# Performance work log

Measured on AMD Instinct MI355X. Metric: run time of the kernel, lower is better.

## Reference

```python
import jax, jax.numpy as jnp
import numpy as np

B, I, O, T, L = 16, 512, 512, 256, 4096
EPS = 1e-8


def setup_inputs() -> dict:
    key = jax.random.key(0)
    ks = jax.random.split(key, 10)
    def lin_w(k, out_d, in_d):  # kaiming-uniform-ish init like torch Linear
        bound = 1.0 / np.sqrt(in_d)
        return jax.random.uniform(k, (out_d, in_d), jnp.float32, -bound, bound)
    return {
        "x": jax.random.normal(ks[0], (B, I, L), jnp.float32),
        "t": jax.random.normal(ks[1], (B, T), jnp.float32),
        "weight": lin_w(ks[2], O, I),            # base conv weight [O, I]
        "W1": lin_w(ks[3], T, T), "b1": jnp.zeros((T,), jnp.float32),
        "W2": lin_w(ks[4], T, T), "b2": jnp.zeros((T,), jnp.float32),
        "W3": lin_w(ks[5], I, T), "b3": jnp.zeros((I,), jnp.float32),
    }


def reference(x, t, weight, W1, b1, W2, b2, W3, b3):
    # mod MLP: Linear -> SiLU -> Linear -> SiLU -> Linear
    h = jax.nn.silu(t @ W1.T + b1)
    h = jax.nn.silu(h @ W2.T + b2)
    s = h @ W3.T + b3 + 1.0                    # [B, I] modulation scales
    bw = weight[None, :, :] * s[:, None, :]    # [B, O, I]
    demod = jax.lax.rsqrt(jnp.sum(bw * bw, axis=2) + EPS)  # [B, O]
    bw = bw * demod[:, :, None]                # demodulated per-sample weights
    # grouped 1x1 conv (groups=B) == batched pointwise contraction
    return jnp.einsum('boi,bil->bol', bw, x)   # [B, O, L]
```

## Files before the change

kernel.cpp:

```cpp
#include <hip/hip_runtime.h>
#include <hip/hip_bf16.h>

typedef float f4v __attribute__((ext_vector_type(4)));
typedef float f32x4 __attribute__((ext_vector_type(4)));
typedef __bf16 bf16x8 __attribute__((ext_vector_type(8)));

#define GLDS16(gsrc, ldst)                                                  \
  __builtin_amdgcn_global_load_lds(                                         \
      (const __attribute__((address_space(1))) unsigned int*)(gsrc),        \
      (__attribute__((address_space(3))) unsigned int*)(ldst), 16, 0, 0)

__device__ __forceinline__ unsigned pack2bf(float lo, float hi) {
  unsigned short ua = __builtin_bit_cast(unsigned short, (__bf16)lo);
  unsigned short ub = __builtin_bit_cast(unsigned short, (__bf16)hi);
  return (unsigned)ua | ((unsigned)ub << 16);
}

__global__ __launch_bounds__(256) void mlp_kernel(
    const float* __restrict__ t,
    const float* __restrict__ W1, const float* __restrict__ b1,
    const float* __restrict__ W2, const float* __restrict__ b2,
    const float* __restrict__ W3, const float* __restrict__ b3,
    float* __restrict__ s_out) {
  __shared__ float tt[256];
  __shared__ float hh[256];
  const int b = blockIdx.x;
  const int tid = threadIdx.x;
  tt[tid] = t[b * 256 + tid];
  __syncthreads();
  float acc = b1[tid];
  {
    const f4v* wrow = (const f4v*)(W1 + tid * 256);
    #pragma unroll 16
    for (int k = 0; k < 64; ++k) {
      f4v wv = wrow[k];
      acc += wv[0] * tt[4 * k] + wv[1] * tt[4 * k + 1] +
             wv[2] * tt[4 * k + 2] + wv[3] * tt[4 * k + 3];
    }
  }
  float h = acc / (1.0f + expf(-acc));
  __syncthreads();
  hh[tid] = h;
  __syncthreads();
  acc = b2[tid];
  {
    const f4v* wrow = (const f4v*)(W2 + tid * 256);
    #pragma unroll 16
    for (int k = 0; k < 64; ++k) {
      f4v wv = wrow[k];
      acc += wv[0] * hh[4 * k] + wv[1] * hh[4 * k + 1] +
             wv[2] * hh[4 * k + 2] + wv[3] * hh[4 * k + 3];
    }
  }
  h = acc / (1.0f + expf(-acc));
  __syncthreads();
  tt[tid] = h;
  __syncthreads();
  #pragma unroll
  for (int rep = 0; rep < 2; ++rep) {
    const int o = rep * 256 + tid;
    float a3 = b3[o];
    const f4v* wrow = (const f4v*)(W3 + o * 256);
    #pragma unroll 16
    for (int k = 0; k < 64; ++k) {
      f4v wv = wrow[k];
      a3 += wv[0] * tt[4 * k] + wv[1] * tt[4 * k + 1] +
            wv[2] * tt[4 * k + 2] + wv[3] * tt[4 * k + 3];
    }
    s_out[b * 512 + o] = a3 + 1.0f;
  }
}

__global__ __launch_bounds__(256) void modw_kernel(
    const float* __restrict__ weight, const float* __restrict__ s_in,
    unsigned short* __restrict__ bwq) {
  const int tid = threadIdx.x;
  const int wid = (blockIdx.x << 2) | (tid >> 6);
  const int b = wid >> 9;
  const int o = wid & 511;
  const int lane = tid & 63;
  const f4v* wp = (const f4v*)(weight + o * 512 + lane * 8);
  const f4v* sp = (const f4v*)(s_in + b * 512 + lane * 8);
  f4v w0 = wp[0], w1 = wp[1];
  f4v s0 = sp[0], s1 = sp[1];
  float p[8];
  p[0] = w0[0] * s0[0]; p[1] = w0[1] * s0[1];
  p[2] = w0[2] * s0[2]; p[3] = w0[3] * s0[3];
  p[4] = w1[0] * s1[0]; p[5] = w1[1] * s1[1];
  p[6] = w1[2] * s1[2]; p[7] = w1[3] * s1[3];
  float ss = 0.0f;
  #pragma unroll
  for (int i = 0; i < 8; ++i) ss += p[i] * p[i];
  #pragma unroll
  for (int off = 32; off; off >>= 1) ss += __shfl_xor(ss, off);
  const float d = rsqrtf(ss + 1e-8f);
  uint4 outw;
  outw.x = pack2bf(p[0] * d, p[1] * d);
  outw.y = pack2bf(p[2] * d, p[3] * d);
  outw.z = pack2bf(p[4] * d, p[5] * d);
  outw.w = pack2bf(p[6] * d, p[7] * d);
  *(uint4*)(bwq + ((size_t)(b * 512 + o)) * 512 + lane * 8) = outw;
}

__global__ __launch_bounds__(256, 3) void gemm_kernel(
    const float* __restrict__ x, const unsigned short* __restrict__ bwq,
    float* __restrict__ out) {
  __shared__ __align__(16) unsigned short As[3][128 * 32];
  __shared__ __align__(16) unsigned short Bs[2][128 * 32];

  const int bid = blockIdx.x;
  const int swz = ((bid & 7) << 8) | (bid >> 3);
  const int mt = swz & 3;
  const int nt = (swz >> 2) & 31;
  const int bb = swz >> 7;

  const int tid = threadIdx.x;
  const int lane = tid & 63;
  const int wv = tid >> 6;
  const int wr = wv >> 1, wc = wv & 1;

  const unsigned short* abase = bwq + ((size_t)(bb * 512 + mt * 128)) * 512;
  const float* xbase = x + ((size_t)bb * 512) * 4096 + nt * 128;

  const int pq = tid >> 5;
  const int lc = tid & 31;
  const float* xp = xbase + (size_t)(pq * 4) * 4096 + lc * 4;
  const int sw_w = (lc & 3) << 4;
  char* BsB = (char*)Bs;

  const int g0 = tid, g1 = 256 + tid;
  const unsigned short* asrc0 = abase + (g0 >> 2) * 512 + (g0 & 3) * 8;
  const unsigned short* asrc1 = abase + (g1 >> 2) * 512 + (g1 & 3) * 8;

  const int arow = wr * 64 + (lane & 15);
  const int kgo = (lane >> 4) * 8;
  const int nrow0 = wc * 64 + (lane & 15);
  const int sb = (nrow0 >> 2) & 3;
  const int bByte = nrow0 * 64 + (((lane >> 4) ^ sb) << 4);

  f32x4 acc[4][4] = {};
  f4v xv[3][4];

#define LOADX(SET, STEP)                                                    \
  do {                                                                      \
    const float* _p = xp + (size_t)((STEP) * 32) * 4096;                    \
    xv[SET][0] = *(const f4v*)(_p);                                         \
    xv[SET][1] = *(const f4v*)(_p + 4096);                                  \
    xv[SET][2] = *(const f4v*)(_p + 8192);                                  \
    xv[SET][3] = *(const f4v*)(_p + 12288);                                 \
  } while (0)

#define STAGEA(STEP, BUF)                                                   \
  do {                                                                      \
    GLDS16(asrc0 + (STEP) * 32, &As[BUF][g0 * 8]);                          \
    GLDS16(asrc1 + (STEP) * 32, &As[BUF][g1 * 8]);                          \
  } while (0)

#define PACKB(SET, BUF)                                                     \
  do {                                                                      \
    char* _bs = BsB + (BUF) * 8192;                                         \
    _Pragma("unroll")                                                       \
    for (int j = 0; j < 4; ++j) {                                           \
      uint2 val;                                                            \
      val.x = pack2bf(xv[SET][0][j], xv[SET][1][j]);                        \
      val.y = pack2bf(xv[SET][2][j], xv[SET][3][j]);                        \
      const int n = (lc << 2) + j;                                          \
      *(uint2*)(_bs + n * 64 + ((pq * 8) ^ sw_w)) = val;                    \
    }                                                                       \
  } while (0)

#define FENCE() asm volatile("" ::: "memory")
#define BARN(N)                                                             \
  do {                                                                      \
    asm volatile("s_waitcnt lgkmcnt(0)\n\ts_waitcnt vmcnt(" #N ")" :::      \
                     "memory");                                             \
    __builtin_amdgcn_s_barrier();                                           \
    asm volatile("" ::: "memory");                                          \
  } while (0)

#define COMPUTE(CA, CB)                                                     \
  do {                                                                      \
    const unsigned short* ab = &As[CA][0];                                  \
    const char* bbuf = BsB + (CB) * 8192;                                   \
    bf16x8 a0 = *(const bf16x8*)(ab + arow * 32 + kgo);                     \
    bf16x8 a1 = *(const bf16x8*)(ab + arow * 32 + 512 + kgo);               \
    bf16x8 a2 = *(const bf16x8*)(ab + arow * 32 + 1024 + kgo);              \
    bf16x8 a3 = *(const bf16x8*)(ab + arow * 32 + 1536 + kgo);              \
    bf16x8 bf0 = *(const bf16x8*)(bbuf + bByte);                            \
    bf16x8 bf1 = *(const bf16x8*)(bbuf + bByte + 1024);                     \
    bf16x8 bf2 = *(const bf16x8*)(bbuf + bByte + 2048);                     \
    bf16x8 bf3 = *(const bf16x8*)(bbuf + bByte + 3072);                     \
    acc[0][0] = __builtin_amdgcn_mfma_f32_16x16x32_bf16(a0, bf0, acc[0][0], 0, 0, 0); \
    acc[0][1] = __builtin_amdgcn_mfma_f32_16x16x32_bf16(a0, bf1, acc[0][1], 0, 0, 0); \
    acc[0][2] = __builtin_amdgcn_mfma_f32_16x16x32_bf16(a0, bf2, acc[0][2], 0, 0, 0); \
    acc[0][3] = __builtin_amdgcn_mfma_f32_16x16x32_bf16(a0, bf3, acc[0][3], 0, 0, 0); \
    acc[1][0] = __builtin_amdgcn_mfma_f32_16x16x32_bf16(a1, bf0, acc[1][0], 0, 0, 0); \
    acc[1][1] = __builtin_amdgcn_mfma_f32_16x16x32_bf16(a1, bf1, acc[1][1], 0, 0, 0); \
    acc[1][2] = __builtin_amdgcn_mfma_f32_16x16x32_bf16(a1, bf2, acc[1][2], 0, 0, 0); \
    acc[1][3] = __builtin_amdgcn_mfma_f32_16x16x32_bf16(a1, bf3, acc[1][3], 0, 0, 0); \
    acc[2][0] = __builtin_amdgcn_mfma_f32_16x16x32_bf16(a2, bf0, acc[2][0], 0, 0, 0); \
    acc[2][1] = __builtin_amdgcn_mfma_f32_16x16x32_bf16(a2, bf1, acc[2][1], 0, 0, 0); \
    acc[2][2] = __builtin_amdgcn_mfma_f32_16x16x32_bf16(a2, bf2, acc[2][2], 0, 0, 0); \
    acc[2][3] = __builtin_amdgcn_mfma_f32_16x16x32_bf16(a2, bf3, acc[2][3], 0, 0, 0); \
    acc[3][0] = __builtin_amdgcn_mfma_f32_16x16x32_bf16(a3, bf0, acc[3][0], 0, 0, 0); \
    acc[3][1] = __builtin_amdgcn_mfma_f32_16x16x32_bf16(a3, bf1, acc[3][1], 0, 0, 0); \
    acc[3][2] = __builtin_amdgcn_mfma_f32_16x16x32_bf16(a3, bf2, acc[3][2], 0, 0, 0); \
    acc[3][3] = __builtin_amdgcn_mfma_f32_16x16x32_bf16(a3, bf3, acc[3][3], 0, 0, 0); \
  } while (0)

  STAGEA(0, 0);
  FENCE();
  LOADX(0, 0);
  STAGEA(1, 1);
  FENCE();
  LOADX(1, 1);
  LOADX(2, 2);
  PACKB(0, 0);
  BARN(10);

  #pragma unroll
  for (int it = 0; it < 16; ++it) {
    if (it <= 14) PACKB((it + 1) % 3, (it + 1) & 1);
    if (it <= 13) STAGEA(it + 2, (it + 2) % 3);
    FENCE();
    if (it <= 12) LOADX(it % 3, it + 3);
    COMPUTE(it % 3, it & 1);
    if (it <= 12) {
      BARN(10);
    } else if (it == 13) {
      BARN(6);
    } else if (it == 14) {
      BARN(0);
    }
  }

  const size_t ob =
      ((size_t)(bb * 512 + mt * 128 + wr * 64 + ((lane >> 4) << 2))) * 4096 +
      nt * 128 + wc * 64 + (lane & 15);
  #pragma unroll
  for (int mi = 0; mi < 4; ++mi)
    #pragma unroll
    for (int ni = 0; ni < 4; ++ni)
      #pragma unroll
      for (int jj = 0; jj < 4; ++jj)
        out[ob + (size_t)(mi * 16 + jj) * 4096 + ni * 16] = acc[mi][ni][jj];

#undef LOADX
#undef STAGEA
#undef PACKB
#undef FENCE
#undef BARN
#undef COMPUTE
}

extern "C" void kernel_launch(void* const* d_in, const int* in_sizes, int n_in,
                              void* d_out, int out_size, void* d_ws, size_t ws_size,
                              hipStream_t stream) {
  const float* x      = (const float*)d_in[0];
  const float* t      = (const float*)d_in[1];
  const float* weight = (const float*)d_in[2];
  const float* W1     = (const float*)d_in[3];
  const float* b1     = (const float*)d_in[4];
  const float* W2     = (const float*)d_in[5];
  const float* b2     = (const float*)d_in[6];
  const float* W3     = (const float*)d_in[7];
  const float* b3     = (const float*)d_in[8];
  float* out = (float*)d_out;

  float* s_ws = (float*)d_ws;
  unsigned short* bwq = (unsigned short*)((char*)d_ws + 32 * 1024);

  mlp_kernel<<<16, 256, 0, stream>>>(t, W1, b1, W2, b2, W3, b3, s_ws);
  modw_kernel<<<2048, 256, 0, stream>>>(weight, s_ws, bwq);
  gemm_kernel<<<2048, 256, 0, stream>>>(x, bwq, out);
}
```

Before: 126.4 us.

## Restructure GEMM pipeline with rotating LDS pointers and two-set register prefetch

Replaces the fully unrolled 16-step loop with a 7-iteration, twice-unrolled loop that rotates three A-tile LDS pointers and ping-pongs two named register sets of x values, plus a two-step tail. The hand-tuned vmcnt waits are removed. Barriers now wait only on lgkmcnt and add a sched_barrier, so the compiler has to place the global-load waits itself. The occupancy hint in launch_bounds is also dropped. The aim is less register pressure and code size, but prefetch depth for x falls from three steps to two. Correctness for the asynchronous LDS DMA of A now rests on waits the compiler inserts.

```diff
diff --git a/kernel.cpp b/kernel.cpp
--- a/kernel.cpp
+++ b/kernel.cpp
@@ -102,11 +102,11 @@
   *(uint4*)(bwq + ((size_t)(b * 512 + o)) * 512 + lane * 8) = outw;
 }
 
-__global__ __launch_bounds__(256, 3) void gemm_kernel(
+__global__ __launch_bounds__(256) void gemm_kernel(
     const float* __restrict__ x, const unsigned short* __restrict__ bwq,
     float* __restrict__ out) {
-  __shared__ __align__(16) unsigned short As[3][128 * 32];
-  __shared__ __align__(16) unsigned short Bs[2][128 * 32];
+  __shared__ __align__(16) unsigned short AsBuf[3][128 * 32];
+  __shared__ __align__(16) unsigned short BsBuf[2][128 * 32];
 
   const int bid = blockIdx.x;
   const int swz = ((bid & 7) << 8) | (bid >> 3);
@@ -126,11 +126,12 @@
   const int lc = tid & 31;
   const float* xp = xbase + (size_t)(pq * 4) * 4096 + lc * 4;
   const int sw_w = (lc & 3) << 4;
-  char* BsB = (char*)Bs;
 
   const int g0 = tid, g1 = 256 + tid;
   const unsigned short* asrc0 = abase + (g0 >> 2) * 512 + (g0 & 3) * 8;
   const unsigned short* asrc1 = abase + (g1 >> 2) * 512 + (g1 & 3) * 8;
+  const int aoff0 = g0 * 8;
+  const int aoff1 = g1 * 8;
 
   const int arow = wr * 64 + (lane & 15);
   const int kgo = (lane >> 4) * 8;
@@ -139,57 +140,60 @@
   const int bByte = nrow0 * 64 + (((lane >> 4) ^ sb) << 4);
 
   f32x4 acc[4][4] = {};
-  f4v xv[3][4];
-
-#define LOADX(SET, STEP)                                                    \
+
+  f4v xa0, xa1, xa2, xa3, xb0, xb1, xb2, xb3;
+
+  unsigned short* pA0 = &AsBuf[0][0];
+  unsigned short* pA1 = &AsBuf[1][0];
+  unsigned short* pA2 = &AsBuf[2][0];
+  char* bs0 = (char*)&BsBuf[0][0];
+  char* bs1 = (char*)&BsBuf[1][0];
+
+#define LOADX(R0, R1, R2, R3, STEP)                                         \
   do {                                                                      \
     const float* _p = xp + (size_t)((STEP) * 32) * 4096;                    \
-    xv[SET][0] = *(const f4v*)(_p);                                         \
-    xv[SET][1] = *(const f4v*)(_p + 4096);                                  \
-    xv[SET][2] = *(const f4v*)(_p + 8192);                                  \
-    xv[SET][3] = *(const f4v*)(_p + 12288);                                 \
-  } while (0)
-
-#define STAGEA(STEP, BUF)                                                   \
-  do {                                                                      \
-    GLDS16(asrc0 + (STEP) * 32, &As[BUF][g0 * 8]);                          \
-    GLDS16(asrc1 + (STEP) * 32, &As[BUF][g1 * 8]);                          \
-  } while (0)
-
-#define PACKB(SET, BUF)                                                     \
-  do {                                                                      \
-    char* _bs = BsB + (BUF) * 8192;                                         \
+    R0 = *(const f4v*)(_p);                                                 \
+    R1 = *(const f4v*)(_p + 4096);                                          \
+    R2 = *(const f4v*)(_p + 8192);                                          \
+    R3 = *(const f4v*)(_p + 12288);                                         \
+  } while (0)
+
+#define STAGEA(STEP, PDST)                                                  \
+  do {                                                                      \
+    GLDS16(asrc0 + (STEP) * 32, (PDST) + aoff0);                            \
+    GLDS16(asrc1 + (STEP) * 32, (PDST) + aoff1);                            \
+  } while (0)
+
+#define PACKB(R0, R1, R2, R3, BSP)                                          \
+  do {                                                                      \
     _Pragma("unroll")                                                       \
     for (int j = 0; j < 4; ++j) {                                           \
       uint2 val;                                                            \
-      val.x = pack2bf(xv[SET][0][j], xv[SET][1][j]);                        \
-      val.y = pack2bf(xv[SET][2][j], xv[SET][3][j]);                        \
+      val.x = pack2bf(R0[j], R1[j]);                                        \
+      val.y = pack2bf(R2[j], R3[j]);                                        \
       const int n = (lc << 2) + j;                                          \
-      *(uint2*)(_bs + n * 64 + ((pq * 8) ^ sw_w)) = val;                    \
+      *(uint2*)((BSP) + n * 64 + ((pq * 8) ^ sw_w)) = val;                  \
     }                                                                       \
   } while (0)
 
-#define FENCE() asm volatile("" ::: "memory")
-#define BARN(N)                                                             \
-  do {                                                                      \
-    asm volatile("s_waitcnt lgkmcnt(0)\n\ts_waitcnt vmcnt(" #N ")" :::      \
-                     "memory");                                             \
+#define BAR()                                                               \
+  do {                                                                      \
+    asm volatile("s_waitcnt lgkmcnt(0)" ::: "memory");                      \
     __builtin_amdgcn_s_barrier();                                           \
-    asm volatile("" ::: "memory");                                          \
-  } while (0)
-
-#define COMPUTE(CA, CB)                                                     \
-  do {                                                                      \
-    const unsigned short* ab = &As[CA][0];                                  \
-    const char* bbuf = BsB + (CB) * 8192;                                   \
+    __builtin_amdgcn_sched_barrier(0);                                      \
+  } while (0)
+
+#define COMPUTE(PA, BSP)                                                    \
+  do {                                                                      \
+    const unsigned short* ab = (PA);                                        \
     bf16x8 a0 = *(const bf16x8*)(ab + arow * 32 + kgo);                     \
     bf16x8 a1 = *(const bf16x8*)(ab + arow * 32 + 512 + kgo);               \
     bf16x8 a2 = *(const bf16x8*)(ab + arow * 32 + 1024 + kgo);              \
     bf16x8 a3 = *(const bf16x8*)(ab + arow * 32 + 1536 + kgo);              \
-    bf16x8 bf0 = *(const bf16x8*)(bbuf + bByte);                            \
-    bf16x8 bf1 = *(const bf16x8*)(bbuf + bByte + 1024);                     \
-    bf16x8 bf2 = *(const bf16x8*)(bbuf + bByte + 2048);                     \
-    bf16x8 bf3 = *(const bf16x8*)(bbuf + bByte + 3072);                     \
+    bf16x8 bf0 = *(const bf16x8*)((BSP) + bByte);                           \
+    bf16x8 bf1 = *(const bf16x8*)((BSP) + bByte + 1024);                    \
+    bf16x8 bf2 = *(const bf16x8*)((BSP) + bByte + 2048);                    \
+    bf16x8 bf3 = *(const bf16x8*)((BSP) + bByte + 3072);                    \
     acc[0][0] = __builtin_amdgcn_mfma_f32_16x16x32_bf16(a0, bf0, acc[0][0], 0, 0, 0); \
     acc[0][1] = __builtin_amdgcn_mfma_f32_16x16x32_bf16(a0, bf1, acc[0][1], 0, 0, 0); \
     acc[0][2] = __builtin_amdgcn_mfma_f32_16x16x32_bf16(a0, bf2, acc[0][2], 0, 0, 0); \
@@ -208,31 +212,36 @@
     acc[3][3] = __builtin_amdgcn_mfma_f32_16x16x32_bf16(a3, bf3, acc[3][3], 0, 0, 0); \
   } while (0)
 
-  STAGEA(0, 0);
-  FENCE();
-  LOADX(0, 0);
-  STAGEA(1, 1);
-  FENCE();
-  LOADX(1, 1);
-  LOADX(2, 2);
-  PACKB(0, 0);
-  BARN(10);
-
-  #pragma unroll
-  for (int it = 0; it < 16; ++it) {
-    if (it <= 14) PACKB((it + 1) % 3, (it + 1) & 1);
-    if (it <= 13) STAGEA(it + 2, (it + 2) % 3);
-    FENCE();
-    if (it <= 12) LOADX(it % 3, it + 3);
-    COMPUTE(it % 3, it & 1);
-    if (it <= 12) {
-      BARN(10);
-    } else if (it == 13) {
-      BARN(6);
-    } else if (it == 14) {
-      BARN(0);
-    }
-  }
+#define ROT()                                                               \
+  do { unsigned short* _t = pA0; pA0 = pA1; pA1 = pA2; pA2 = _t; } while (0)
+
+  STAGEA(0, pA0);
+  LOADX(xa0, xa1, xa2, xa3, 0);
+  STAGEA(1, pA1);
+  LOADX(xb0, xb1, xb2, xb3, 1);
+
+  for (int it2 = 0; it2 < 7; ++it2) {
+    const int it = it2 * 2;
+    PACKB(xa0, xa1, xa2, xa3, bs0);
+    STAGEA(it + 2, pA2);
+    LOADX(xa0, xa1, xa2, xa3, it + 2);
+    BAR();
+    COMPUTE(pA0, bs0);
+    ROT();
+    PACKB(xb0, xb1, xb2, xb3, bs1);
+    STAGEA(it + 3, pA2);
+    LOADX(xb0, xb1, xb2, xb3, it + 3);
+    BAR();
+    COMPUTE(pA0, bs1);
+    ROT();
+  }
+  PACKB(xa0, xa1, xa2, xa3, bs0);
+  BAR();
+  COMPUTE(pA0, bs0);
+  ROT();
+  PACKB(xb0, xb1, xb2, xb3, bs1);
+  BAR();
+  COMPUTE(pA0, bs1);
 
   const size_t ob =
       ((size_t)(bb * 512 + mt * 128 + wr * 64 + ((lane >> 4) << 2))) * 4096 +
@@ -248,9 +257,9 @@
 #undef LOADX
 #undef STAGEA
 #undef PACKB
-#undef FENCE
-#undef BARN
+#undef BAR
 #undef COMPUTE
+#undef ROT
 }
 
 extern "C" void kernel_launch(void* const* d_in, const int* in_sizes, int n_in,
```

New measurement: 127.9 us. No clear change (+1.2%).
